# Optimization experiments

Hardware: AMD Instinct MI355X
Metric: run time of the kernel (lower is better)

Reference implementation:

```python
import jax, jax.numpy as jnp
import numpy as np

LN_EPS = 1e-5

def _ln(x, g, b):
    mu = jnp.mean(x, axis=-1, keepdims=True)
    var = jnp.mean((x - mu) ** 2, axis=-1, keepdims=True)
    return (x - mu) / jnp.sqrt(var + LN_EPS) * g + b

def setup_inputs() -> dict:
    key = jax.random.key(0)
    ks = jax.random.split(key, 8)
    b, h, n, e, pd = 8, 8, 4096, 64, 16  # pd = d // 4
    inp = {
        "x": jax.random.normal(ks[0], (b, h, n, e), dtype=jnp.float32),
        "W0": jax.random.normal(ks[1], (1, pd), dtype=jnp.float32) * 0.5,
        "b0": jnp.zeros((pd,), jnp.float32),
        "g1": jnp.ones((pd,), jnp.float32),
        "be1": jnp.zeros((pd,), jnp.float32),
        "W1": jax.random.normal(ks[2], (pd, pd), dtype=jnp.float32) * 0.25,
        "b1": jnp.zeros((pd,), jnp.float32),
        "g2": jnp.ones((pd,), jnp.float32),
        "be2": jnp.zeros((pd,), jnp.float32),
        "W2": jax.random.normal(ks[3], (pd, pd), dtype=jnp.float32) * 0.25,
        "b2": jnp.zeros((pd,), jnp.float32),
        "g3": jnp.ones((pd,), jnp.float32),
        "be3": jnp.zeros((pd,), jnp.float32),
        "W3": jax.random.normal(ks[4], (pd, h), dtype=jnp.float32) * 0.25,
        "b3": jnp.zeros((h,), jnp.float32),
    }
    return inp

def _dpb(t, W0, b0, g1, be1, W1, b1, g2, be2, W2, b2, g3, be3, W3, b3):
    # DynamicPosBiasV2, non-residual: pos3(pos2(pos1(pos_proj(t))))
    hdd = t @ W0 + b0                       # (m, pd)
    hdd = jax.nn.relu(_ln(hdd, g1, be1)) @ W1 + b1
    hdd = jax.nn.relu(_ln(hdd, g2, be2)) @ W2 + b2
    return jax.nn.relu(_ln(hdd, g3, be3)) @ W3 + b3  # (m, h)

def reference(x, W0, b0, g1, be1, W1, b1, g2, be2, W2, b2, g3, be3, W3, b3):
    n = x.shape[-2]
    p = (W0, b0, g1, be1, W1, b1, g2, be2, W2, b2, g3, be3, W3, b3)
    zero = _dpb(jnp.zeros((1, 1), x.dtype), *p).T          # (h, 1)
    pos = _dpb(jnp.arange(1, n, dtype=x.dtype)[:, None], *p).T   # (h, n-1)
    neg_idx = -jnp.arange(n - 1, 0, -1, dtype=x.dtype)[:, None]  # [-(n-1),...,-1]
    neg = _dpb(neg_idx, *p).T                              # (h, n-1)
    a = jnp.concatenate([zero, pos, zero, neg], axis=-1)   # (h, 2n)
    # circular conv of length 2n along seq dim -2
    y = jnp.fft.rfft(x, n=2 * n, axis=-2)                  # (b, h, n+1, e) complex
    v = jnp.fft.rfft(a, axis=-1)[None, :, :, None]         # (1, h, n+1, 1)
    out = jnp.fft.irfft(v * y, n=2 * n, axis=-2)[:, :, :n, :]
    return out
```

## Files before the change

### kernel.cpp

```cpp
#include <hip/hip_runtime.h>
#include <math.h>

#define NSEQ 4096
#define LFFT 8192
#define NT   512

__device__ __forceinline__ float2 cadd(float2 a, float2 b){ return make_float2(a.x+b.x, a.y+b.y); }
__device__ __forceinline__ float2 csub(float2 a, float2 b){ return make_float2(a.x-b.x, a.y-b.y); }
__device__ __forceinline__ float2 cmul(float2 a, float2 b){
  return make_float2(fmaf(a.x,b.x,-(a.y*b.y)), fmaf(a.x,b.y, a.y*b.x));
}
__device__ __forceinline__ float2 cmulc(float2 a, float2 b){
  return make_float2(fmaf(a.x,b.x, a.y*b.y), fmaf(a.y,b.x,-(a.x*b.y)));
}
#define R8C 0.70710678118654752440f
__device__ __forceinline__ float2 mulW8p1(float2 z){ return make_float2(R8C*(z.x+z.y), R8C*(z.y-z.x)); }
__device__ __forceinline__ float2 mulW8p3(float2 z){ return make_float2(R8C*(z.y-z.x), -R8C*(z.x+z.y)); }
__device__ __forceinline__ float2 mulW8m1(float2 z){ return make_float2(R8C*(z.x-z.y), R8C*(z.x+z.y)); }
__device__ __forceinline__ float2 mulW8m3(float2 z){ return make_float2(-R8C*(z.x+z.y), R8C*(z.x-z.y)); }
__device__ __forceinline__ float2 mulmi(float2 z){ return make_float2( z.y, -z.x); }
__device__ __forceinline__ float2 mulpi(float2 z){ return make_float2(-z.y,  z.x); }

__device__ __forceinline__ int swz(int p){ return p ^ ((p>>4)&15); }

__device__ __forceinline__ float2 twget(const float2* twHi, const float2* twLo, int k){
  return cmul(twHi[k>>6], twLo[k&63]);
}

__device__ __forceinline__ void init_tw(float2* twHi, float2* twLo){
  const float PI2 = 6.28318530717958647692f;
  int tid = threadIdx.x;
  if (tid < 128){
    float ang = -PI2 * (float)(tid*64) / (float)LFFT;
    float s, c; sincosf(ang, &s, &c);
    twHi[tid] = make_float2(c, s);
  } else if (tid < 192){
    int k = tid - 128;
    float ang = -PI2 * (float)k / (float)LFFT;
    float s, c; sincosf(ang, &s, &c);
    twLo[k] = make_float2(c, s);
  }
  __syncthreads();
}

template<int H>
__device__ __forceinline__ void fwd_r8(float2* z, const float2* twHi, const float2* twLo){
  constexpr int STEP = LFFT/(8*H);
  const int tid = threadIdx.x;
  #pragma unroll
  for (int r = 0; r < LFFT/8/NT; ++r){
    int i = r*NT + tid;
    int pos = i & (H-1);
    int base = ((i - pos) << 3) + pos;
    float2 x0 = z[swz(base)];
    float2 x1 = z[swz(base+H)];
    float2 x2 = z[swz(base+2*H)];
    float2 x3 = z[swz(base+3*H)];
    float2 x4 = z[swz(base+4*H)];
    float2 x5 = z[swz(base+5*H)];
    float2 x6 = z[swz(base+6*H)];
    float2 x7 = z[swz(base+7*H)];
    float2 e0=cadd(x0,x4), o0=csub(x0,x4);
    float2 e1=cadd(x1,x5), o1=csub(x1,x5);
    float2 e2=cadd(x2,x6), o2=csub(x2,x6);
    float2 e3=cadd(x3,x7), o3=csub(x3,x7);
    float2 ta=cadd(e0,e2), tb=csub(e0,e2);
    float2 tc=cadd(e1,e3), td=csub(e1,e3);
    float2 y0=cadd(ta,tc), y4=csub(ta,tc);
    float2 y2=make_float2(tb.x+td.y, tb.y-td.x);
    float2 y6=make_float2(tb.x-td.y, tb.y+td.x);
    o1 = mulW8p1(o1); o2 = mulmi(o2); o3 = mulW8p3(o3);
    float2 ua=cadd(o0,o2), ub=csub(o0,o2);
    float2 uc=cadd(o1,o3), ud=csub(o1,o3);
    float2 y1=cadd(ua,uc), y5=csub(ua,uc);
    float2 y3=make_float2(ub.x+ud.y, ub.y-ud.x);
    float2 y7=make_float2(ub.x-ud.y, ub.y+ud.x);
    z[swz(base)] = y0;
    if constexpr (H > 1){
      float2 w1 = twget(twHi,twLo, pos*STEP);
      float2 w2 = cmul(w1,w1);
      float2 w3 = cmul(w2,w1);
      float2 w4 = cmul(w2,w2);
      float2 w5 = cmul(w4,w1);
      float2 w6 = cmul(w4,w2);
      float2 w7 = cmul(w4,w3);
      z[swz(base+H)]   = cmul(y1,w1);
      z[swz(base+2*H)] = cmul(y2,w2);
      z[swz(base+3*H)] = cmul(y3,w3);
      z[swz(base+4*H)] = cmul(y4,w4);
      z[swz(base+5*H)] = cmul(y5,w5);
      z[swz(base+6*H)] = cmul(y6,w6);
      z[swz(base+7*H)] = cmul(y7,w7);
    } else {
      z[swz(base+H)]   = y1;
      z[swz(base+2*H)] = y2;
      z[swz(base+3*H)] = y3;
      z[swz(base+4*H)] = y4;
      z[swz(base+5*H)] = y5;
      z[swz(base+6*H)] = y6;
      z[swz(base+7*H)] = y7;
    }
  }
  __syncthreads();
}

template<int H>
__device__ __forceinline__ void inv_r8(float2* z, const float2* twHi, const float2* twLo){
  constexpr int STEP = LFFT/(8*H);
  const int tid = threadIdx.x;
  #pragma unroll
  for (int r = 0; r < LFFT/8/NT; ++r){
    int i = r*NT + tid;
    int pos = i & (H-1);
    int base = ((i - pos) << 3) + pos;
    float2 x0 = z[swz(base)];
    float2 x1,x2,x3,x4,x5,x6,x7;
    if constexpr (H > 1){
      float2 w1 = twget(twHi,twLo, pos*STEP);
      float2 w2 = cmul(w1,w1);
      float2 w3 = cmul(w2,w1);
      float2 w4 = cmul(w2,w2);
      float2 w5 = cmul(w4,w1);
      float2 w6 = cmul(w4,w2);
      float2 w7 = cmul(w4,w3);
      x1 = cmulc(z[swz(base+H)],   w1);
      x2 = cmulc(z[swz(base+2*H)], w2);
      x3 = cmulc(z[swz(base+3*H)], w3);
      x4 = cmulc(z[swz(base+4*H)], w4);
      x5 = cmulc(z[swz(base+5*H)], w5);
      x6 = cmulc(z[swz(base+6*H)], w6);
      x7 = cmulc(z[swz(base+7*H)], w7);
    } else {
      x1 = z[swz(base+H)];
      x2 = z[swz(base+2*H)];
      x3 = z[swz(base+3*H)];
      x4 = z[swz(base+4*H)];
      x5 = z[swz(base+5*H)];
      x6 = z[swz(base+6*H)];
      x7 = z[swz(base+7*H)];
    }
    float2 e0=cadd(x0,x4), o0=csub(x0,x4);
    float2 e1=cadd(x1,x5), o1=csub(x1,x5);
    float2 e2=cadd(x2,x6), o2=csub(x2,x6);
    float2 e3=cadd(x3,x7), o3=csub(x3,x7);
    float2 ta=cadd(e0,e2), tb=csub(e0,e2);
    float2 tc=cadd(e1,e3), td=csub(e1,e3);
    float2 y0=cadd(ta,tc), y4=csub(ta,tc);
    float2 y2=make_float2(tb.x-td.y, tb.y+td.x);
    float2 y6=make_float2(tb.x+td.y, tb.y-td.x);
    o1 = mulW8m1(o1); o2 = mulpi(o2); o3 = mulW8m3(o3);
    float2 ua=cadd(o0,o2), ub=csub(o0,o2);
    float2 uc=cadd(o1,o3), ud=csub(o1,o3);
    float2 y1=cadd(ua,uc), y5=csub(ua,uc);
    float2 y3=make_float2(ub.x-ud.y, ub.y+ud.x);
    float2 y7=make_float2(ub.x+ud.y, ub.y-ud.x);
    z[swz(base)]     = y0;
    z[swz(base+H)]   = y1;
    z[swz(base+2*H)] = y2;
    z[swz(base+3*H)] = y3;
    z[swz(base+4*H)] = y4;
    z[swz(base+5*H)] = y5;
    z[swz(base+6*H)] = y6;
    z[swz(base+7*H)] = y7;
  }
  __syncthreads();
}

__device__ __forceinline__ void ln_relu16(const float* v, float* y, const float* g, const float* be){
  float mu = 0.f;
  #pragma unroll
  for (int p=0;p<16;++p) mu += v[p];
  mu *= (1.f/16.f);
  float var = 0.f;
  #pragma unroll
  for (int p=0;p<16;++p){ float d = v[p]-mu; var = fmaf(d,d,var); }
  var *= (1.f/16.f);
  float inv = 1.f / sqrtf(var + 1e-5f);
  #pragma unroll
  for (int p=0;p<16;++p){
    float t = fmaf((v[p]-mu)*inv, g[p], be[p]);
    y[p] = t > 0.f ? t : 0.f;
  }
}

__global__ void dpb_kernel(const float* __restrict__ W0, const float* __restrict__ b0,
                           const float* __restrict__ g1, const float* __restrict__ be1,
                           const float* __restrict__ W1, const float* __restrict__ b1,
                           const float* __restrict__ g2, const float* __restrict__ be2,
                           const float* __restrict__ W2, const float* __restrict__ b2,
                           const float* __restrict__ g3, const float* __restrict__ be3,
                           const float* __restrict__ W3, const float* __restrict__ b3,
                           float* __restrict__ a){
  int j = blockIdx.x*256 + threadIdx.x;
  float t;
  if (j == 0 || j == NSEQ) t = 0.f;
  else if (j < NSEQ)       t = (float)j;
  else                     t = (float)(j - LFFT);

  float v[16], y[16];
  #pragma unroll
  for (int p=0;p<16;++p) v[p] = fmaf(t, W0[p], b0[p]);
  ln_relu16(v, y, g1, be1);
  #pragma unroll
  for (int q=0;q<16;++q){ float s=b1[q];
    #pragma unroll
    for (int p=0;p<16;++p) s = fmaf(y[p], W1[p*16+q], s);
    v[q]=s; }
  ln_relu16(v, y, g2, be2);
  #pragma unroll
  for (int q=0;q<16;++q){ float s=b2[q];
    #pragma unroll
    for (int p=0;p<16;++p) s = fmaf(y[p], W2[p*16+q], s);
    v[q]=s; }
  ln_relu16(v, y, g3, be3);
  #pragma unroll
  for (int hh=0;hh<8;++hh){ float s=b3[hh];
    #pragma unroll
    for (int p=0;p<16;++p) s = fmaf(y[p], W3[p*8+hh], s);
    a[hh*LFFT + j] = s; }
}

__global__ __launch_bounds__(NT, 4) void afft_kernel(const float* __restrict__ a,
                                                     float2* __restrict__ Ahat){
  __shared__ float2 z[LFFT];
  __shared__ float2 twHi[128];
  __shared__ float2 twLo[64];
  init_tw(twHi, twLo);
  const int h = blockIdx.x, tid = threadIdx.x;
  const float* ah = a + h*LFFT;
  #pragma unroll
  for (int r = 0; r < LFFT/NT; ++r){
    int j = r*NT + tid;
    z[swz(j)] = make_float2(ah[j], 0.f);
  }
  __syncthreads();
  #pragma unroll
  for (int r = 0; r < LFFT/2/NT; ++r){
    int i = r*NT + tid;
    float2 u = z[swz(i)], v = z[swz(i+NSEQ)];
    z[swz(i)]      = cadd(u, v);
    z[swz(i+NSEQ)] = cmul(csub(u, v), twget(twHi,twLo,i));
  }
  __syncthreads();
  fwd_r8<512>(z,twHi,twLo); fwd_r8<64>(z,twHi,twLo);
  fwd_r8<8>(z,twHi,twLo);   fwd_r8<1>(z,twHi,twLo);
  const float sc = 1.f/(float)LFFT;
  float2* Ah = Ahat + h*LFFT;
  #pragma unroll
  for (int r = 0; r < LFFT/NT; ++r){
    int p = r*NT + tid;
    float2 v = z[swz(p)];
    Ah[p] = make_float2(v.x*sc, v.y*sc);
  }
}

__global__ __launch_bounds__(NT, 4) void conv_kernel(const float* __restrict__ x,
                                                     const float2* __restrict__ Ahat,
                                                     float* __restrict__ out){
  __shared__ float2 z[LFFT];
  __shared__ float2 twHi[128];
  __shared__ float2 twLo[64];
  init_tw(twHi, twLo);

  int bid = blockIdx.x;
  int logical = (bid & 7)*256 + (bid >> 3);
  int bh   = logical >> 5;
  int pair = logical & 31;
  int h    = bh & 7;
  const int tid = threadIdx.x;

  const float2* xp = (const float2*)x + (size_t)bh*NSEQ*32 + pair;
  #pragma unroll
  for (int r = 0; r < NSEQ/NT; ++r){
    int s = r*NT + tid;
    float2 v = xp[(size_t)s*32];
    z[swz(s)]      = v;
    z[swz(s+NSEQ)] = cmul(v, twget(twHi,twLo,s));
  }
  __syncthreads();

  fwd_r8<512>(z,twHi,twLo); fwd_r8<64>(z,twHi,twLo);
  fwd_r8<8>(z,twHi,twLo);   fwd_r8<1>(z,twHi,twLo);

  const float2* Ah = Ahat + h*LFFT;
  #pragma unroll
  for (int r = 0; r < LFFT/NT; ++r){
    int p = r*NT + tid;
    z[swz(p)] = cmul(z[swz(p)], Ah[p]);
  }
  __syncthreads();

  inv_r8<1>(z,twHi,twLo);   inv_r8<8>(z,twHi,twLo);
  inv_r8<64>(z,twHi,twLo);  inv_r8<512>(z,twHi,twLo);

  float2* op = (float2*)out + (size_t)bh*NSEQ*32 + pair;
  #pragma unroll
  for (int r = 0; r < NSEQ/NT; ++r){
    int i = r*NT + tid;
    float2 u = z[swz(i)];
    float2 v = cmulc(z[swz(i+NSEQ)], twget(twHi,twLo,i));
    op[(size_t)i*32] = cadd(u, v);
  }
}

extern "C" void kernel_launch(void* const* d_in, const int* in_sizes, int n_in,
                              void* d_out, int out_size, void* d_ws, size_t ws_size,
                              hipStream_t stream){
  const float* x   = (const float*)d_in[0];
  const float* W0  = (const float*)d_in[1];
  const float* b0  = (const float*)d_in[2];
  const float* g1  = (const float*)d_in[3];
  const float* be1 = (const float*)d_in[4];
  const float* W1  = (const float*)d_in[5];
  const float* b1  = (const float*)d_in[6];
  const float* g2  = (const float*)d_in[7];
  const float* be2 = (const float*)d_in[8];
  const float* W2  = (const float*)d_in[9];
  const float* b2  = (const float*)d_in[10];
  const float* g3  = (const float*)d_in[11];
  const float* be3 = (const float*)d_in[12];
  const float* W3  = (const float*)d_in[13];
  const float* b3  = (const float*)d_in[14];

  float*  a    = (float*)d_ws;
  float2* Ahat = (float2*)((char*)d_ws + (size_t)8*LFFT*sizeof(float));
  float*  outp = (float*)d_out;

  dpb_kernel<<<LFFT/256, 256, 0, stream>>>(W0,b0,g1,be1,W1,b1,g2,be2,W2,b2,g3,be3,W3,b3, a);
  afft_kernel<<<8, NT, 0, stream>>>(a, Ahat);
  conv_kernel<<<2048, NT, 0, stream>>>(x, Ahat, outp);
}
```

Baseline: 110.6 us.

## Fuse spectral multiply into last forward radix-8 pass and double block size

Fuses the pointwise multiply by the precomputed filter spectrum into the final forward radix-8 FFT pass, which removes one full shared-memory read/write sweep and one barrier per block. Threads per block double from 512 to 1024, so each thread handles one butterfly per pass, and the launch-bounds occupancy hint rises from 4 to 8. The butterfly code is factored into helper functions. The filter read in the fused pass is strided by 8 per thread, so global loads are less coalesced, and the larger blocks may raise register pressure.

```diff
diff --git a/kernel.cpp b/kernel.cpp
--- a/kernel.cpp
+++ b/kernel.cpp
@@ -3,7 +3,7 @@
 
 #define NSEQ 4096
 #define LFFT 8192
-#define NT   512
+#define NT   1024
 
 __device__ __forceinline__ float2 cadd(float2 a, float2 b){ return make_float2(a.x+b.x, a.y+b.y); }
 __device__ __forceinline__ float2 csub(float2 a, float2 b){ return make_float2(a.x-b.x, a.y-b.y); }
@@ -43,6 +43,48 @@
   __syncthreads();
 }
 
+struct F2x8 { float2 v0,v1,v2,v3,v4,v5,v6,v7; };
+
+__device__ __forceinline__ F2x8 bfly8_fwd(F2x8 x){
+  float2 e0=cadd(x.v0,x.v4), o0=csub(x.v0,x.v4);
+  float2 e1=cadd(x.v1,x.v5), o1=csub(x.v1,x.v5);
+  float2 e2=cadd(x.v2,x.v6), o2=csub(x.v2,x.v6);
+  float2 e3=cadd(x.v3,x.v7), o3=csub(x.v3,x.v7);
+  float2 ta=cadd(e0,e2), tb=csub(e0,e2);
+  float2 tc=cadd(e1,e3), td=csub(e1,e3);
+  F2x8 y;
+  y.v0=cadd(ta,tc); y.v4=csub(ta,tc);
+  y.v2=make_float2(tb.x+td.y, tb.y-td.x);
+  y.v6=make_float2(tb.x-td.y, tb.y+td.x);
+  o1 = mulW8p1(o1); o2 = mulmi(o2); o3 = mulW8p3(o3);
+  float2 ua=cadd(o0,o2), ub=csub(o0,o2);
+  float2 uc=cadd(o1,o3), ud=csub(o1,o3);
+  y.v1=cadd(ua,uc); y.v5=csub(ua,uc);
+  y.v3=make_float2(ub.x+ud.y, ub.y-ud.x);
+  y.v7=make_float2(ub.x-ud.y, ub.y+ud.x);
+  return y;
+}
+
+__device__ __forceinline__ F2x8 bfly8_inv(F2x8 x){
+  float2 e0=cadd(x.v0,x.v4), o0=csub(x.v0,x.v4);
+  float2 e1=cadd(x.v1,x.v5), o1=csub(x.v1,x.v5);
+  float2 e2=cadd(x.v2,x.v6), o2=csub(x.v2,x.v6);
+  float2 e3=cadd(x.v3,x.v7), o3=csub(x.v3,x.v7);
+  float2 ta=cadd(e0,e2), tb=csub(e0,e2);
+  float2 tc=cadd(e1,e3), td=csub(e1,e3);
+  F2x8 y;
+  y.v0=cadd(ta,tc); y.v4=csub(ta,tc);
+  y.v2=make_float2(tb.x-td.y, tb.y+td.x);
+  y.v6=make_float2(tb.x+td.y, tb.y-td.x);
+  o1 = mulW8m1(o1); o2 = mulpi(o2); o3 = mulW8m3(o3);
+  float2 ua=cadd(o0,o2), ub=csub(o0,o2);
+  float2 uc=cadd(o1,o3), ud=csub(o1,o3);
+  y.v1=cadd(ua,uc); y.v5=csub(ua,uc);
+  y.v3=make_float2(ub.x-ud.y, ub.y+ud.x);
+  y.v7=make_float2(ub.x+ud.y, ub.y-ud.x);
+  return y;
+}
+
 template<int H>
 __device__ __forceinline__ void fwd_r8(float2* z, const float2* twHi, const float2* twLo){
   constexpr int STEP = LFFT/(8*H);
@@ -52,30 +94,13 @@
     int i = r*NT + tid;
     int pos = i & (H-1);
     int base = ((i - pos) << 3) + pos;
-    float2 x0 = z[swz(base)];
-    float2 x1 = z[swz(base+H)];
-    float2 x2 = z[swz(base+2*H)];
-    float2 x3 = z[swz(base+3*H)];
-    float2 x4 = z[swz(base+4*H)];
-    float2 x5 = z[swz(base+5*H)];
-    float2 x6 = z[swz(base+6*H)];
-    float2 x7 = z[swz(base+7*H)];
-    float2 e0=cadd(x0,x4), o0=csub(x0,x4);
-    float2 e1=cadd(x1,x5), o1=csub(x1,x5);
-    float2 e2=cadd(x2,x6), o2=csub(x2,x6);
-    float2 e3=cadd(x3,x7), o3=csub(x3,x7);
-    float2 ta=cadd(e0,e2), tb=csub(e0,e2);
-    float2 tc=cadd(e1,e3), td=csub(e1,e3);
-    float2 y0=cadd(ta,tc), y4=csub(ta,tc);
-    float2 y2=make_float2(tb.x+td.y, tb.y-td.x);
-    float2 y6=make_float2(tb.x-td.y, tb.y+td.x);
-    o1 = mulW8p1(o1); o2 = mulmi(o2); o3 = mulW8p3(o3);
-    float2 ua=cadd(o0,o2), ub=csub(o0,o2);
-    float2 uc=cadd(o1,o3), ud=csub(o1,o3);
-    float2 y1=cadd(ua,uc), y5=csub(ua,uc);
-    float2 y3=make_float2(ub.x+ud.y, ub.y-ud.x);
-    float2 y7=make_float2(ub.x-ud.y, ub.y+ud.x);
-    z[swz(base)] = y0;
+    F2x8 x;
+    x.v0 = z[swz(base)];     x.v1 = z[swz(base+H)];
+    x.v2 = z[swz(base+2*H)]; x.v3 = z[swz(base+3*H)];
+    x.v4 = z[swz(base+4*H)]; x.v5 = z[swz(base+5*H)];
+    x.v6 = z[swz(base+6*H)]; x.v7 = z[swz(base+7*H)];
+    F2x8 y = bfly8_fwd(x);
+    z[swz(base)] = y.v0;
     if constexpr (H > 1){
       float2 w1 = twget(twHi,twLo, pos*STEP);
       float2 w2 = cmul(w1,w1);
@@ -84,22 +109,46 @@
       float2 w5 = cmul(w4,w1);
       float2 w6 = cmul(w4,w2);
       float2 w7 = cmul(w4,w3);
-      z[swz(base+H)]   = cmul(y1,w1);
-      z[swz(base+2*H)] = cmul(y2,w2);
-      z[swz(base+3*H)] = cmul(y3,w3);
-      z[swz(base+4*H)] = cmul(y4,w4);
-      z[swz(base+5*H)] = cmul(y5,w5);
-      z[swz(base+6*H)] = cmul(y6,w6);
-      z[swz(base+7*H)] = cmul(y7,w7);
+      z[swz(base+H)]   = cmul(y.v1,w1);
+      z[swz(base+2*H)] = cmul(y.v2,w2);
+      z[swz(base+3*H)] = cmul(y.v3,w3);
+      z[swz(base+4*H)] = cmul(y.v4,w4);
+      z[swz(base+5*H)] = cmul(y.v5,w5);
+      z[swz(base+6*H)] = cmul(y.v6,w6);
+      z[swz(base+7*H)] = cmul(y.v7,w7);
     } else {
-      z[swz(base+H)]   = y1;
-      z[swz(base+2*H)] = y2;
-      z[swz(base+3*H)] = y3;
-      z[swz(base+4*H)] = y4;
-      z[swz(base+5*H)] = y5;
-      z[swz(base+6*H)] = y6;
-      z[swz(base+7*H)] = y7;
+      z[swz(base+H)]   = y.v1;
+      z[swz(base+2*H)] = y.v2;
+      z[swz(base+3*H)] = y.v3;
+      z[swz(base+4*H)] = y.v4;
+      z[swz(base+5*H)] = y.v5;
+      z[swz(base+6*H)] = y.v6;
+      z[swz(base+7*H)] = y.v7;
     }
+  }
+  __syncthreads();
+}
+
+__device__ __forceinline__ void fwd_r8_mulA(float2* z, const float2* __restrict__ Ah){
+  const int tid = threadIdx.x;
+  #pragma unroll
+  for (int r = 0; r < LFFT/8/NT; ++r){
+    int i = r*NT + tid;
+    int base = i << 3;
+    F2x8 x;
+    x.v0 = z[swz(base)];   x.v1 = z[swz(base+1)];
+    x.v2 = z[swz(base+2)]; x.v3 = z[swz(base+3)];
+    x.v4 = z[swz(base+4)]; x.v5 = z[swz(base+5)];
+    x.v6 = z[swz(base+6)]; x.v7 = z[swz(base+7)];
+    F2x8 y = bfly8_fwd(x);
+    z[swz(base)]   = cmul(y.v0, Ah[base]);
+    z[swz(base+1)] = cmul(y.v1, Ah[base+1]);
+    z[swz(base+2)] = cmul(y.v2, Ah[base+2]);
+    z[swz(base+3)] = cmul(y.v3, Ah[base+3]);
+    z[swz(base+4)] = cmul(y.v4, Ah[base+4]);
+    z[swz(base+5)] = cmul(y.v5, Ah[base+5]);
+    z[swz(base+6)] = cmul(y.v6, Ah[base+6]);
+    z[swz(base+7)] = cmul(y.v7, Ah[base+7]);
   }
   __syncthreads();
 }
@@ -113,8 +162,8 @@
     int i = r*NT + tid;
     int pos = i & (H-1);
     int base = ((i - pos) << 3) + pos;
-    float2 x0 = z[swz(base)];
-    float2 x1,x2,x3,x4,x5,x6,x7;
+    F2x8 x;
+    x.v0 = z[swz(base)];
     if constexpr (H > 1){
       float2 w1 = twget(twHi,twLo, pos*STEP);
       float2 w2 = cmul(w1,w1);
@@ -123,45 +172,31 @@
       float2 w5 = cmul(w4,w1);
       float2 w6 = cmul(w4,w2);
       float2 w7 = cmul(w4,w3);
-      x1 = cmulc(z[swz(base+H)],   w1);
-      x2 = cmulc(z[swz(base+2*H)], w2);
-      x3 = cmulc(z[swz(base+3*H)], w3);
-      x4 = cmulc(z[swz(base+4*H)], w4);
-      x5 = cmulc(z[swz(base+5*H)], w5);
-      x6 = cmulc(z[swz(base+6*H)], w6);
-      x7 = cmulc(z[swz(base+7*H)], w7);
+      x.v1 = cmulc(z[swz(base+H)],   w1);
+      x.v2 = cmulc(z[swz(base+2*H)], w2);
+      x.v3 = cmulc(z[swz(base+3*H)], w3);
+      x.v4 = cmulc(z[swz(base+4*H)], w4);
+      x.v5 = cmulc(z[swz(base+5*H)], w5);
+      x.v6 = cmulc(z[swz(base+6*H)], w6);
+      x.v7 = cmulc(z[swz(base+7*H)], w7);
     } else {
-      x1 = z[swz(base+H)];
-      x2 = z[swz(base+2*H)];
-      x3 = z[swz(base+3*H)];
-      x4 = z[swz(base+4*H)];
-      x5 = z[swz(base+5*H)];
-      x6 = z[swz(base+6*H)];
-      x7 = z[swz(base+7*H)];
+      x.v1 = z[swz(base+H)];
+      x.v2 = z[swz(base+2*H)];
+      x.v3 = z[swz(base+3*H)];
+      x.v4 = z[swz(base+4*H)];
+      x.v5 = z[swz(base+5*H)];
+      x.v6 = z[swz(base+6*H)];
+      x.v7 = z[swz(base+7*H)];
     }
-    float2 e0=cadd(x0,x4), o0=csub(x0,x4);
-    float2 e1=cadd(x1,x5), o1=csub(x1,x5);
-    float2 e2=cadd(x2,x6), o2=csub(x2,x6);
-    float2 e3=cadd(x3,x7), o3=csub(x3,x7);
-    float2 ta=cadd(e0,e2), tb=csub(e0,e2);
-    float2 tc=cadd(e1,e3), td=csub(e1,e3);
-    float2 y0=cadd(ta,tc), y4=csub(ta,tc);
-    float2 y2=make_float2(tb.x-td.y, tb.y+td.x);
-    float2 y6=make_float2(tb.x+td.y, tb.y-td.x);
-    o1 = mulW8m1(o1); o2 = mulpi(o2); o3 = mulW8m3(o3);
-    float2 ua=cadd(o0,o2), ub=csub(o0,o2);
-    float2 uc=cadd(o1,o3), ud=csub(o1,o3);
-    float2 y1=cadd(ua,uc), y5=csub(ua,uc);
-    float2 y3=make_float2(ub.x-ud.y, ub.y+ud.x);
-    float2 y7=make_float2(ub.x+ud.y, ub.y-ud.x);
-    z[swz(base)]     = y0;
-    z[swz(base+H)]   = y1;
-    z[swz(base+2*H)] = y2;
-    z[swz(base+3*H)] = y3;
-    z[swz(base+4*H)] = y4;
-    z[swz(base+5*H)] = y5;
-    z[swz(base+6*H)] = y6;
-    z[swz(base+7*H)] = y7;
+    F2x8 y = bfly8_inv(x);
+    z[swz(base)]     = y.v0;
+    z[swz(base+H)]   = y.v1;
+    z[swz(base+2*H)] = y.v2;
+    z[swz(base+3*H)] = y.v3;
+    z[swz(base+4*H)] = y.v4;
+    z[swz(base+5*H)] = y.v5;
+    z[swz(base+6*H)] = y.v6;
+    z[swz(base+7*H)] = y.v7;
   }
   __syncthreads();
 }
@@ -220,7 +255,7 @@
     a[hh*LFFT + j] = s; }
 }
 
-__global__ __launch_bounds__(NT, 4) void afft_kernel(const float* __restrict__ a,
+__global__ __launch_bounds__(NT, 8) void afft_kernel(const float* __restrict__ a,
                                                      float2* __restrict__ Ahat){
   __shared__ float2 z[LFFT];
   __shared__ float2 twHi[128];
@@ -254,7 +289,7 @@
   }
 }
 
-__global__ __launch_bounds__(NT, 4) void conv_kernel(const float* __restrict__ x,
+__global__ __launch_bounds__(NT, 8) void conv_kernel(const float* __restrict__ x,
                                                      const float2* __restrict__ Ahat,
                                                      float* __restrict__ out){
   __shared__ float2 z[LFFT];
@@ -280,15 +315,8 @@
   __syncthreads();
 
   fwd_r8<512>(z,twHi,twLo); fwd_r8<64>(z,twHi,twLo);
-  fwd_r8<8>(z,twHi,twLo);   fwd_r8<1>(z,twHi,twLo);
-
-  const float2* Ah = Ahat + h*LFFT;
-  #pragma unroll
-  for (int r = 0; r < LFFT/NT; ++r){
-    int p = r*NT + tid;
-    z[swz(p)] = cmul(z[swz(p)], Ah[p]);
-  }
-  __syncthreads();
+  fwd_r8<8>(z,twHi,twLo);
+  fwd_r8_mulA(z, Ahat + h*LFFT);
 
   inv_r8<1>(z,twHi,twLo);   inv_r8<8>(z,twHi,twLo);
   inv_r8<64>(z,twHi,twLo);  inv_r8<512>(z,twHi,twLo);
```

Result: slower. 159.7 us (+44.3%).
